# Kernel optimization log

Hardware: AMD Instinct MI355X
Metric: run time of the kernel (lower is better)

## Reference

```python
import jax, jax.numpy as jnp
import numpy as np

E = 8          # num_experts
K = 2          # top_k
R = 16         # lora_r
SCALING = 32.0 / 16.0  # lora_alpha / lora_r

B, S, H, I = 2, 2048, 2048, 8192


def setup_inputs() -> dict:
    key = jax.random.key(0)
    ks = jax.random.split(key, 11)
    inv_h = 1.0 / np.sqrt(H)
    inv_i = 1.0 / np.sqrt(I)
    return {
        "x": jax.random.normal(ks[0], (B, S, H), jnp.float32),
        "gate_W": jax.random.normal(ks[1], (I, H), jnp.float32) * inv_h,
        "up_W": jax.random.normal(ks[2], (I, H), jnp.float32) * inv_h,
        "down_W": jax.random.normal(ks[3], (H, I), jnp.float32) * inv_i,
        "router_W": jax.random.normal(ks[4], (E, H), jnp.float32) * 0.02,
        "gate_A": jax.random.normal(ks[5], (E, R, H), jnp.float32) * inv_h,
        "gate_B": jax.random.normal(ks[6], (E, I, R), jnp.float32) * 0.01,
        "up_A": jax.random.normal(ks[7], (E, R, H), jnp.float32) * inv_h,
        "up_B": jax.random.normal(ks[8], (E, I, R), jnp.float32) * 0.01,
        "down_A": jax.random.normal(ks[9], (E, R, I), jnp.float32) * inv_i,
        "down_B": jax.random.normal(ks[10], (E, H, R), jnp.float32) * 0.01,
    }


def _mixlora_forward(x, gate_W, up_W, down_W, router_W,
                     gate_A, gate_B, up_A, up_B, down_A, down_B):
    b, s, h = x.shape
    T = b * s
    xf = x.reshape(T, h)                                  # [T, H]

    # Shared base FFN projections (computed once for all experts)
    gate_out = xf @ gate_W.T                              # [T, I]
    up_out = xf @ up_W.T                                  # [T, I]

    # Router: softmax in fp32, top-k, renormalize selected weights
    logits = xf @ router_W.T                              # [T, E]
    probs = jax.nn.softmax(logits.astype(jnp.float32), axis=-1)
    w, idx = jax.lax.top_k(probs, K)                      # [T, K]
    w = w / jnp.sum(w, axis=-1, keepdims=True)

    # Dense per-(token, expert) combine weights; 0 for unselected experts
    onehot = jax.nn.one_hot(idx, E, dtype=probs.dtype)    # [T, K, E]
    w_dense = jnp.einsum('tke,tk->te', onehot, w)         # [T, E]

    # Load-balance aux loss: N * sum_i f_i * P_i
    f_i = jnp.sum(onehot, axis=(0, 1)) / T
    p_i = jnp.mean(probs, axis=0)
    aux_loss = E * jnp.dot(f_i, p_i)

    # Scan over experts, accumulating weighted intermediate and down-delta.
    # Since down_proj is linear, sum_k w_k * down(inter_k) = down(sum_k w_k * inter_k).
    def step(carry, p):
        acc_int, acc_dd = carry
        gA, gB, uA, uB, dA, dB, we = p                    # we: [T]
        gd = ((xf @ gA.T) @ gB.T) * SCALING               # [T, I]
        ud = ((xf @ uA.T) @ uB.T) * SCALING               # [T, I]
        inter = jax.nn.silu(gate_out + gd) * (up_out + ud)  # SwiGLU intermediate
        dd = ((inter @ dA.T) @ dB.T) * SCALING            # [T, H]
        we = we.astype(xf.dtype)[:, None]
        return (acc_int + we * inter, acc_dd + we * dd), None

    init = (jnp.zeros((T, gate_W.shape[0]), xf.dtype),
            jnp.zeros((T, h), xf.dtype))
    (acc_int, acc_dd), _ = jax.lax.scan(
        step, init, (gate_A, gate_B, up_A, up_B, down_A, down_B, w_dense.T))

    out = acc_int @ down_W.T + acc_dd                     # [T, H]
    return out.reshape(b, s, h), aux_loss


def reference(x, gate_W, up_W, down_W, router_W,
              gate_A, gate_B, up_A, up_B, down_A, down_B):
    return _mixlora_forward(x, gate_W, up_W, down_W, router_W,
                            gate_A, gate_B, up_A, up_B, down_A, down_B)
```

## Files before the change

### kernel.cpp

```cpp
#include <hip/hip_runtime.h>
#include <stdint.h>
#include <stddef.h>

#define DEVINL __device__ __forceinline__

typedef short sv8 __attribute__((ext_vector_type(8)));
typedef unsigned short usv8 __attribute__((ext_vector_type(8)));
typedef unsigned short usv4 __attribute__((ext_vector_type(4)));
typedef float f32x4 __attribute__((ext_vector_type(4)));

constexpr int T_TOK = 4096;
constexpr int H_DIM = 2048;
constexpr int I_DIM = 8192;
constexpr int E_NUM = 8;
constexpr int R_LORA = 16;
constexpr float SCALING = 2.0f;
constexpr int NQ = 4;
constexpr int TQ = T_TOK / NQ;
constexpr int PQ = TQ * 2;
constexpr int P_TOT = T_TOK * 2;

DEVINL float bf2f(unsigned short u) {
  union { uint32_t i; float f; } v; v.i = ((uint32_t)u) << 16; return v.f;
}
DEVINL unsigned short f2bf(float x) {
  union { float f; uint32_t i; } v; v.f = x;
  uint32_t r = v.i + 0x7FFFu + ((v.i >> 16) & 1u);
  return (unsigned short)(r >> 16);
}
DEVINL float bflo(uint32_t w) {
  union { uint32_t i; float f; } v; v.i = w << 16; return v.f;
}
DEVINL float bfhi(uint32_t w) {
  union { uint32_t i; float f; } v; v.i = w & 0xFFFF0000u; return v.f;
}

DEVINL f32x4 MFMA_BF16(sv8 a, sv8 b, f32x4 c) {
  return __builtin_amdgcn_mfma_f32_16x16x32_bf16(a, b, c, 0, 0, 0);
}

DEVINL void load16_to_lds(const void* g, void* l) {
  __builtin_amdgcn_global_load_lds(
      (const __attribute__((address_space(1))) uint32_t*)g,
      (__attribute__((address_space(3))) uint32_t*)l, 16, 0, 0);
}

#define BARRIER() __builtin_amdgcn_s_barrier()
#define SB0() __builtin_amdgcn_sched_barrier(0)
#define LGKM0() asm volatile("s_waitcnt lgkmcnt(0)" ::: "memory")

__global__ void cast_f32_to_bf16(const float4* __restrict__ src, usv4* __restrict__ dst) {
  long i = (long)blockIdx.x * blockDim.x + threadIdx.x;
  float4 v = src[i];
  usv4 o;
  o[0] = f2bf(v.x); o[1] = f2bf(v.y); o[2] = f2bf(v.z); o[3] = f2bf(v.w);
  dst[i] = o;
}

__global__ void zero_lcnt(int* lcnt) {
  if (threadIdx.x < E_NUM * NQ) lcnt[threadIdx.x] = 0;
}

__global__ void router_kernel(const float* __restrict__ x, const float* __restrict__ rW,
                              float* __restrict__ wbuf, int* __restrict__ idxb,
                              float* __restrict__ probs, int* __restrict__ lcnt,
                              int* __restrict__ lists, unsigned short* __restrict__ xf_bf) {
  const int wave = threadIdx.x >> 6, lane = threadIdx.x & 63;
  const int t = blockIdx.x * 4 + wave;
  const float* xr = x + (long)t * H_DIM;
  unsigned short* xbr = xf_bf + (long)t * H_DIM;
  float acc[E_NUM];
#pragma unroll
  for (int e = 0; e < E_NUM; ++e) acc[e] = 0.f;
  for (int h = lane; h < H_DIM; h += 64) {
    float xv = xr[h];
    xbr[h] = f2bf(xv);
#pragma unroll
    for (int e = 0; e < E_NUM; ++e) acc[e] += xv * rW[e * H_DIM + h];
  }
#pragma unroll
  for (int e = 0; e < E_NUM; ++e) {
#pragma unroll
    for (int off = 32; off; off >>= 1) acc[e] += __shfl_xor(acc[e], off);
  }
  if (lane == 0) {
    float mx = acc[0];
#pragma unroll
    for (int e = 1; e < E_NUM; ++e) mx = fmaxf(mx, acc[e]);
    float p[E_NUM];
    float s = 0.f;
#pragma unroll
    for (int e = 0; e < E_NUM; ++e) { p[e] = expf(acc[e] - mx); s += p[e]; }
    float inv = 1.f / s;
#pragma unroll
    for (int e = 0; e < E_NUM; ++e) p[e] *= inv;
    int e1 = 0;
    for (int e = 1; e < E_NUM; ++e) if (p[e] > p[e1]) e1 = e;
    int e2 = (e1 == 0) ? 1 : 0;
    for (int e = 0; e < E_NUM; ++e) if (e != e1 && p[e] > p[e2]) e2 = e;
    float w1 = p[e1], w2 = p[e2], wsum = w1 + w2;
    wbuf[t * 2 + 0] = w1 / wsum;
    wbuf[t * 2 + 1] = w2 / wsum;
    idxb[t * 2 + 0] = e1;
    idxb[t * 2 + 1] = e2;
#pragma unroll
    for (int e = 0; e < E_NUM; ++e) probs[(long)t * E_NUM + e] = p[e];
    const int q = t / TQ;
    int p1 = atomicAdd(&lcnt[e1 * NQ + q], 1); lists[(e1 * NQ + q) * TQ + p1] = t * 2 + 0;
    int p2 = atomicAdd(&lcnt[e2 * NQ + q], 1); lists[(e2 * NQ + q) * TQ + p2] = t * 2 + 1;
  }
}

__global__ void aux_kernel(const float* __restrict__ probs, const int* __restrict__ lcnt,
                           float* __restrict__ aux_out) {
  const int lane = threadIdx.x;
  float s[E_NUM];
#pragma unroll
  for (int e = 0; e < E_NUM; ++e) s[e] = 0.f;
  for (int t = lane; t < T_TOK; t += 64) {
#pragma unroll
    for (int e = 0; e < E_NUM; ++e) s[e] += probs[(long)t * E_NUM + e];
  }
#pragma unroll
  for (int e = 0; e < E_NUM; ++e) {
#pragma unroll
    for (int off = 32; off; off >>= 1) s[e] += __shfl_xor(s[e], off);
  }
  if (lane == 0) {
    float a = 0.f;
#pragma unroll
    for (int e = 0; e < E_NUM; ++e) {
      int cnt = 0;
#pragma unroll
      for (int q = 0; q < NQ; ++q) cnt += lcnt[e * NQ + q];
      a += ((float)cnt / (float)T_TOK) * (s[e] / (float)T_TOK);
    }
    *aux_out = (float)E_NUM * a;
  }
}

__global__ __launch_bounds__(256)
void lora_a_mfma_kernel(const unsigned short* __restrict__ xf_bf,
                        const unsigned short* __restrict__ gA_bf,
                        const unsigned short* __restrict__ uA_bf,
                        const int* __restrict__ lists, const int* __restrict__ lcnt,
                        float* __restrict__ vg, float* __restrict__ vu) {
  const int q = blockIdx.x / (E_NUM * 16);
  const int rem = blockIdx.x % (E_NUM * 16);
  const int e = rem >> 4;
  const int wave = threadIdx.x >> 6, lane = threadIdx.x & 63;
  const int grp = (rem & 15) * 4 + wave;
  const int npairs = lcnt[e * NQ + q];
  if (grp * 16 >= npairs) return;
  const int* lst = lists + (e * NQ + q) * TQ;
  const int slot = lane & 15;
  int pidx = grp * 16 + slot;
  int pair = lst[(pidx < npairs) ? pidx : grp * 16];
  int t = pair >> 1;
  const long kb = (long)blockIdx.y * 1024 + (lane >> 4) * 8;
  const unsigned short* arow = xf_bf + (long)t * H_DIM + kb;
  const unsigned short* bg = gA_bf + ((long)e * R_LORA + slot) * H_DIM + kb;
  const unsigned short* bu = uA_bf + ((long)e * R_LORA + slot) * H_DIM + kb;
  f32x4 ag = {}, au = {};
#pragma unroll 4
  for (int k = 0; k < 1024; k += 32) {
    sv8 a = *(const sv8*)(arow + k);
    ag = MFMA_BF16(a, *(const sv8*)(bg + k), ag);
    au = MFMA_BF16(a, *(const sv8*)(bu + k), au);
  }
  const int orow = (lane >> 4) * 4;
  const long base = (long)blockIdx.y * P_TOT;
#pragma unroll
  for (int rg = 0; rg < 4; ++rg) {
    int pidx2 = grp * 16 + orow + rg;
    if (pidx2 < npairs) {
      int pr = lst[pidx2];
      vg[(base + pr) * R_LORA + slot] = ag[rg];
      vu[(base + pr) * R_LORA + slot] = au[rg];
    }
  }
}

__global__ void reduce_uguu_kernel(const float* __restrict__ vg, const float* __restrict__ vu,
                                   float* __restrict__ ug, float* __restrict__ uu) {
  long i = (long)blockIdx.x * 256 + threadIdx.x;
  ug[i] = vg[i] + vg[(long)P_TOT * R_LORA + i];
  uu[i] = vu[i] + vu[(long)P_TOT * R_LORA + i];
}

__global__ __launch_bounds__(512, 2)
void gemm8p_kernel(const unsigned short* __restrict__ A,
                   const unsigned short* __restrict__ B0,
                   const unsigned short* __restrict__ B1,
                   unsigned short* __restrict__ C0,
                   unsigned short* __restrict__ C1,
                   int K, int ldc) {
  extern __shared__ unsigned short lds[];
  const unsigned short* __restrict__ B = blockIdx.z ? B1 : B0;
  unsigned short* __restrict__ C = blockIdx.z ? C1 : C0;
  const int tid = threadIdx.x;
  const int wave = tid >> 6, lane = tid & 63;
  const int wm = wave >> 2, wn = wave & 3;
  const long m0 = (long)blockIdx.y * 256;
  const long n0 = (long)blockIdx.x * 256;
  const int NT = K >> 6;

  const int lr = lane & 15;
  const int lc = (lane >> 4) * 8;
  const int xm = ((lane & 4) << 3) | ((lane & 2) << 3) | ((lane & 1) << 6);
  const int srow = tid >> 3;
  const int scol = (tid & 7) * 8;
  const int gcol = scol ^ (((tid >> 5) & 1) << 4) ^ (((tid >> 4) & 1) << 3)
                        ^ (((tid >> 3) & 1) << 5);

  f32x4 acc[8][4] = {};
  sv8 aF[4][2], bF[4][2];

  auto ldsAt = [&](int buf, int mat) -> unsigned short* {
    return lds + (((buf << 1) + mat) << 14);
  };
  auto stageA = [&](int buf, int R, long k0) {
    load16_to_lds(A + (m0 + R + srow) * K + k0 + gcol,
                  ldsAt(buf, 0) + ((R + srow) << 6) + scol);
  };
  auto stageB = [&](int buf, int R, long k0) {
    load16_to_lds(B + (n0 + R + srow) * K + k0 + gcol,
                  ldsAt(buf, 1) + ((R + srow) << 6) + scol);
  };
  auto rdA = [&](int buf, int row16, int ks) -> sv8 {
    int bo = ((((row16 + lr) << 7) + ((ks * 32 + lc) << 1))) ^ xm;
    return *(const sv8*)((const char*)ldsAt(buf, 0) + bo);
  };
  auto rdB = [&](int buf, int row16, int ks) -> sv8 {
    int bo = ((((row16 + lr) << 7) + ((ks * 32 + lc) << 1))) ^ xm;
    return *(const sv8*)((const char*)ldsAt(buf, 1) + bo);
  };

  stageA(0, 0, 0); stageA(0, 64, 0); stageA(0, 128, 0); stageA(0, 192, 0);
  stageB(0, 0, 0); stageB(0, 64, 0); stageB(0, 128, 0); stageB(0, 192, 0);
  if (NT > 1) {
    stageA(1, 0, 64); stageA(1, 128, 64);
    asm volatile("s_waitcnt vmcnt(2)" ::: "memory");
  } else {
    asm volatile("s_waitcnt vmcnt(0)" ::: "memory");
  }
  BARRIER();

  for (int t = 0; t < NT; ++t) {
    const int P = t & 1, Q = P ^ 1;
    const long kQ = ((long)t + 1) << 6;
    const long kP2 = ((long)t + 2) << 6;
    const bool hQ = (t + 1) < NT, hP2 = (t + 2) < NT;

#pragma unroll
    for (int mf = 0; mf < 4; ++mf)
#pragma unroll
      for (int ks = 0; ks < 2; ++ks)
        aF[mf][ks] = rdA(P, wm * 128 + mf * 16, ks);
#pragma unroll
    for (int nf = 0; nf < 2; ++nf)
#pragma unroll
      for (int ks = 0; ks < 2; ++ks)
        bF[nf][ks] = rdB(P, wn * 64 + nf * 16, ks);
    if (hQ) { stageA(Q, 64, kQ); stageA(Q, 192, kQ); }
    BARRIER(); LGKM0(); SB0();
    __builtin_amdgcn_s_setprio(1);
#pragma unroll
    for (int mf = 0; mf < 4; ++mf)
#pragma unroll
      for (int nf = 0; nf < 2; ++nf)
#pragma unroll
        for (int ks = 0; ks < 2; ++ks)
          acc[mf][nf] = MFMA_BF16(aF[mf][ks], bF[nf][ks], acc[mf][nf]);
    __builtin_amdgcn_s_setprio(0);
    BARRIER();

#pragma unroll
    for (int nf = 0; nf < 2; ++nf)
#pragma unroll
      for (int ks = 0; ks < 2; ++ks)
        bF[2 + nf][ks] = rdB(P, wn * 64 + (2 + nf) * 16, ks);
    if (hQ) { stageB(Q, 0, kQ); stageB(Q, 64, kQ); }
    BARRIER(); LGKM0(); SB0();
    __builtin_amdgcn_s_setprio(1);
#pragma unroll
    for (int mf = 0; mf < 4; ++mf)
#pragma unroll
      for (int nf = 0; nf < 2; ++nf)
#pragma unroll
        for (int ks = 0; ks < 2; ++ks)
          acc[mf][2 + nf] = MFMA_BF16(aF[mf][ks], bF[2 + nf][ks], acc[mf][2 + nf]);
    __builtin_amdgcn_s_setprio(0);
    BARRIER();

#pragma unroll
    for (int mf = 0; mf < 4; ++mf)
#pragma unroll
      for (int ks = 0; ks < 2; ++ks)
        aF[mf][ks] = rdA(P, wm * 128 + 64 + mf * 16, ks);
    if (hQ) { stageB(Q, 128, kQ); stageB(Q, 192, kQ); }
    BARRIER(); LGKM0(); SB0();
    __builtin_amdgcn_s_setprio(1);
#pragma unroll
    for (int mf = 0; mf < 4; ++mf)
#pragma unroll
      for (int nf = 0; nf < 2; ++nf)
#pragma unroll
        for (int ks = 0; ks < 2; ++ks)
          acc[4 + mf][nf] = MFMA_BF16(aF[mf][ks], bF[nf][ks], acc[4 + mf][nf]);
    __builtin_amdgcn_s_setprio(0);
    BARRIER();

    if (hP2) {
      stageA(P, 0, kP2); stageA(P, 128, kP2);
      asm volatile("s_waitcnt vmcnt(2)" ::: "memory");
    } else {
      asm volatile("s_waitcnt vmcnt(0)" ::: "memory");
    }
    BARRIER(); LGKM0(); SB0();
    __builtin_amdgcn_s_setprio(1);
#pragma unroll
    for (int mf = 0; mf < 4; ++mf)
#pragma unroll
      for (int nf = 0; nf < 2; ++nf)
#pragma unroll
        for (int ks = 0; ks < 2; ++ks)
          acc[4 + mf][2 + nf] = MFMA_BF16(aF[mf][ks], bF[2 + nf][ks], acc[4 + mf][2 + nf]);
    __builtin_amdgcn_s_setprio(0);
    BARRIER();
  }

  const int rb = (lane >> 4) * 4, cb = lane & 15;
#pragma unroll
  for (int mf = 0; mf < 8; ++mf)
#pragma unroll
    for (int nf = 0; nf < 4; ++nf) {
      long col = n0 + wn * 64 + nf * 16 + cb;
#pragma unroll
      for (int r = 0; r < 4; ++r) {
        long row = m0 + wm * 128 + mf * 16 + rb + r;
        C[row * ldc + col] = f2bf(acc[mf][nf][r]);
      }
    }
}

__global__ __launch_bounds__(256)
void combine2_kernel(const unsigned short* __restrict__ g_bf,
                     const unsigned short* __restrict__ u_bf,
                     const float* __restrict__ gB, const float* __restrict__ uB,
                     const float* __restrict__ ug, const float* __restrict__ uu,
                     const float* __restrict__ wbuf,
                     const int* __restrict__ lists, const int* __restrict__ lcnt,
                     unsigned short* __restrict__ winter, int q) {
  const int e = blockIdx.y >> 4, chunk = blockIdx.y & 15;
  const int npairs = lcnt[e * NQ + q];
  const int pbase = chunk * 64;
  if (pbase >= npairs) return;
  const int wave = threadIdx.x >> 6, lane = threadIdx.x & 63;
  const long i0 = (long)blockIdx.x * 256 + lane * 4;
  uint32_t gbp[32], ubp[32];
#pragma unroll
  for (int j = 0; j < 4; ++j) {
    const float4* gp = (const float4*)(gB + ((long)e * I_DIM + i0 + j) * R_LORA);
    const float4* up = (const float4*)(uB + ((long)e * I_DIM + i0 + j) * R_LORA);
#pragma unroll
    for (int c = 0; c < 4; ++c) {
      float4 gv = gp[c], uv = up[c];
      gbp[j * 8 + c * 2 + 0] = (uint32_t)f2bf(gv.x) | ((uint32_t)f2bf(gv.y) << 16);
      gbp[j * 8 + c * 2 + 1] = (uint32_t)f2bf(gv.z) | ((uint32_t)f2bf(gv.w) << 16);
      ubp[j * 8 + c * 2 + 0] = (uint32_t)f2bf(uv.x) | ((uint32_t)f2bf(uv.y) << 16);
      ubp[j * 8 + c * 2 + 1] = (uint32_t)f2bf(uv.z) | ((uint32_t)f2bf(uv.w) << 16);
    }
  }
  for (int pl = 0; pl < 16; ++pl) {
    int pi = pbase + wave + pl * 4;
    if (pi >= npairs) break;
    int pair = lists[(e * NQ + q) * TQ + pi];
    int t = pair >> 1, plocal = pair - q * PQ;
    float w = wbuf[pair];
    const float2* ug2 = (const float2*)(ug + (long)pair * R_LORA);
    const float2* uu2 = (const float2*)(uu + (long)pair * R_LORA);
    usv4 gv = *(const usv4*)(g_bf + (long)t * I_DIM + i0);
    usv4 uv = *(const usv4*)(u_bf + (long)t * I_DIM + i0);
    float gd[4] = {0.f, 0.f, 0.f, 0.f}, ud[4] = {0.f, 0.f, 0.f, 0.f};
#pragma unroll
    for (int c = 0; c < 8; ++c) {
      float2 a = ug2[c], b = uu2[c];
#pragma unroll
      for (int j = 0; j < 4; ++j) {
        uint32_t gw = gbp[j * 8 + c], uw = ubp[j * 8 + c];
        gd[j] += a.x * bflo(gw) + a.y * bfhi(gw);
        ud[j] += b.x * bflo(uw) + b.y * bfhi(uw);
      }
    }
    usv4 o;
#pragma unroll
    for (int j = 0; j < 4; ++j) {
      float zg = bf2f(gv[j]) + SCALING * gd[j];
      float zu = bf2f(uv[j]) + SCALING * ud[j];
      float sil = zg / (1.f + __expf(-zg));
      o[j] = f2bf(w * sil * zu);
    }
    *(usv4*)(winter + (long)plocal * I_DIM + i0) = o;
  }
}

__global__ void acc_kernel(const unsigned short* __restrict__ winter,
                           unsigned short* __restrict__ acc_bf, int q) {
  long gid = (long)blockIdx.x * 256 + threadIdx.x;
  int tl = (int)(gid >> 10);
  int ig = (int)(gid & 1023);
  int t = q * TQ + tl;
  usv8 a = *(const usv8*)(winter + ((long)(tl * 2 + 0)) * I_DIM + ig * 8);
  usv8 b = *(const usv8*)(winter + ((long)(tl * 2 + 1)) * I_DIM + ig * 8);
  usv8 o;
#pragma unroll
  for (int j = 0; j < 8; ++j) o[j] = f2bf(bf2f(a[j]) + bf2f(b[j]));
  *(usv8*)(acc_bf + (long)t * I_DIM + ig * 8) = o;
}

__global__ __launch_bounds__(256)
void lorav_mfma_kernel(const unsigned short* __restrict__ winter,
                       const unsigned short* __restrict__ dA_bf,
                       const int* __restrict__ lists, const int* __restrict__ lcnt,
                       float* __restrict__ vv, int q) {
  const int e = blockIdx.x >> 4;
  const int wave = threadIdx.x >> 6, lane = threadIdx.x & 63;
  const int grp = (blockIdx.x & 15) * 4 + wave;
  const int npairs = lcnt[e * NQ + q];
  if (grp * 16 >= npairs) return;
  const int* lst = lists + (e * NQ + q) * TQ;
  const int slot = lane & 15;
  int pidx = grp * 16 + slot;
  int pair = lst[(pidx < npairs) ? pidx : grp * 16];
  int plocal = pair - q * PQ;
  const long kb = (long)blockIdx.y * 1024 + (lane >> 4) * 8;
  const unsigned short* arow = winter + (long)plocal * I_DIM + kb;
  const unsigned short* brow = dA_bf + ((long)e * R_LORA + slot) * I_DIM + kb;
  f32x4 acc = {};
#pragma unroll 4
  for (int k = 0; k < 1024; k += 32)
    acc = MFMA_BF16(*(const sv8*)(arow + k), *(const sv8*)(brow + k), acc);
  const int orow = (lane >> 4) * 4;
  const long base = (long)blockIdx.y * P_TOT;
#pragma unroll
  for (int rg = 0; rg < 4; ++rg) {
    int pidx2 = grp * 16 + orow + rg;
    if (pidx2 < npairs) {
      int pr = lst[pidx2];
      vv[(base + pr) * R_LORA + slot] = acc[rg];
    }
  }
}

__global__ void reduce_v_kernel(const float* __restrict__ vv, float* __restrict__ vbuf) {
  long i = (long)blockIdx.x * 256 + threadIdx.x;
  float s = 0.f;
#pragma unroll
  for (int kc = 0; kc < 8; ++kc) s += vv[(long)kc * P_TOT * R_LORA + i];
  vbuf[i] = s;
}

__global__ void dd_kernel(const float* __restrict__ vbuf, const int* __restrict__ idxb,
                          const float* __restrict__ dB,
                          float* __restrict__ out) {
  const int t = blockIdx.y;
  const int h = blockIdx.x * 256 + threadIdx.x;
  const int e0 = idxb[t * 2 + 0], e1 = idxb[t * 2 + 1];
  const float4* v0p = (const float4*)(vbuf + (long)(t * 2 + 0) * R_LORA);
  const float4* v1p = (const float4*)(vbuf + (long)(t * 2 + 1) * R_LORA);
  const float4* b0 = (const float4*)(dB + ((long)e0 * H_DIM + h) * R_LORA);
  const float4* b1 = (const float4*)(dB + ((long)e1 * H_DIM + h) * R_LORA);
  float dd = 0.f;
#pragma unroll
  for (int qq = 0; qq < 4; ++qq) {
    float4 v0 = v0p[qq], x0 = b0[qq];
    float4 v1 = v1p[qq], x1 = b1[qq];
    dd += v0.x * x0.x + v0.y * x0.y + v0.z * x0.z + v0.w * x0.w;
    dd += v1.x * x1.x + v1.y * x1.y + v1.z * x1.z + v1.w * x1.w;
  }
  out[(long)t * H_DIM + h] = SCALING * dd;
}

__global__ __launch_bounds__(256, 2)
void gemm2_kernel(const unsigned short* __restrict__ A,
                  const unsigned short* __restrict__ B,
                  float* __restrict__ out) {
  constexpr int Kd = I_DIM;
  __shared__ unsigned short As[128 * 32];
  __shared__ unsigned short Bs[128 * 32];
  const int tid = threadIdx.x;
  const int wave = tid >> 6, lane = tid & 63;
  const int wm = wave >> 1, wn = wave & 1;
  const long m0 = (long)blockIdx.y * 128;
  const long n0 = (long)blockIdx.x * 128;
  f32x4 acc[4][4] = {};
  const int srow = wave * 32 + (lane >> 2);
  const int scol = (lane & 3) * 8;
  const unsigned short* Ag = A + (m0 + srow) * Kd + scol;
  const unsigned short* Bg = B + (n0 + srow) * Kd + scol;
  const int frA = wm * 64 + (lane & 15);
  const int frB = wn * 64 + (lane & 15);
  const int fc = (lane >> 4) * 8;

  for (int k0 = 0; k0 < Kd; k0 += 32) {
    __syncthreads();
#pragma unroll
    for (int c = 0; c < 2; ++c) {
      load16_to_lds(Ag + (long)c * 16 * Kd + k0, &As[(wave * 32 + c * 16) * 32]);
      load16_to_lds(Bg + (long)c * 16 * Kd + k0, &Bs[(wave * 32 + c * 16) * 32]);
    }
    __syncthreads();
    sv8 af[4], bf[4];
#pragma unroll
    for (int m = 0; m < 4; ++m) af[m] = *(const sv8*)&As[(frA + m * 16) * 32 + fc];
#pragma unroll
    for (int n = 0; n < 4; ++n) bf[n] = *(const sv8*)&Bs[(frB + n * 16) * 32 + fc];
#pragma unroll
    for (int m = 0; m < 4; ++m)
#pragma unroll
      for (int n = 0; n < 4; ++n) acc[m][n] = MFMA_BF16(af[m], bf[n], acc[m][n]);
  }

  const int rb = (lane >> 4) * 4, cb = lane & 15;
#pragma unroll
  for (int m = 0; m < 4; ++m)
#pragma unroll
    for (int n = 0; n < 4; ++n) {
      long col = n0 + wn * 64 + n * 16 + cb;
#pragma unroll
      for (int r = 0; r < 4; ++r) {
        long row = m0 + wm * 64 + m * 16 + rb + r;
        out[row * H_DIM + col] += acc[m][n][r];
      }
    }
}

extern "C" void kernel_launch(void* const* d_in, const int* in_sizes, int n_in,
                              void* d_out, int out_size, void* d_ws, size_t ws_size,
                              hipStream_t stream) {
  (void)in_sizes; (void)n_in; (void)out_size;
  const float* x        = (const float*)d_in[0];
  const float* gate_W   = (const float*)d_in[1];
  const float* up_W     = (const float*)d_in[2];
  const float* down_W   = (const float*)d_in[3];
  const float* router_W = (const float*)d_in[4];
  const float* gate_A   = (const float*)d_in[5];
  const float* gate_B   = (const float*)d_in[6];
  const float* up_A     = (const float*)d_in[7];
  const float* up_B     = (const float*)d_in[8];
  const float* down_A   = (const float*)d_in[9];
  const float* down_B   = (const float*)d_in[10];
  float* out = (float*)d_out;

  char* ws = (char*)d_ws;
  size_t off = 0;
  auto take = [&](size_t bytes) -> char* {
    char* p = ws + off;
    off += (bytes + 255) & ~(size_t)255;
    return p;
  };
  unsigned short* xf_bf  = (unsigned short*)take((size_t)T_TOK * H_DIM * 2);
  unsigned short* gW_bf  = (unsigned short*)take((size_t)I_DIM * H_DIM * 2);
  unsigned short* uW_bf  = (unsigned short*)take((size_t)I_DIM * H_DIM * 2);
  unsigned short* dA_bf  = (unsigned short*)take((size_t)E_NUM * R_LORA * I_DIM * 2);
  unsigned short* g_bf   = (unsigned short*)take((size_t)T_TOK * I_DIM * 2);
  unsigned short* u_bf   = (unsigned short*)take((size_t)T_TOK * I_DIM * 2);
  unsigned short* winterQ= (unsigned short*)take((size_t)PQ * I_DIM * 2);
  float* wbuf  = (float*)take((size_t)P_TOT * 4);
  int*   idxb  = (int*)take((size_t)P_TOT * 4);
  float* ug    = (float*)take((size_t)P_TOT * R_LORA * 4);
  float* uu    = (float*)take((size_t)P_TOT * R_LORA * 4);
  float* vbuf  = (float*)take((size_t)P_TOT * R_LORA * 4);
  float* probs = (float*)take((size_t)T_TOK * E_NUM * 4);
  int*   lcnt  = (int*)take((size_t)E_NUM * NQ * 4);
  int*   lists = (int*)take((size_t)E_NUM * NQ * TQ * 4);

  unsigned short* dW_bf  = gW_bf;
  unsigned short* acc_bf = g_bf;
  float* vg = (float*)winterQ;
  float* vu = (float*)(winterQ + (size_t)1 * 1024 * 1024 / 2);
  unsigned short* gA_bf = winterQ + (size_t)2 * 1024 * 1024 / 2;
  unsigned short* uA_bf = winterQ + (size_t)5 * 512 * 1024 / 2;
  float* vv = (float*)xf_bf;

  if (ws_size < off) return;

  zero_lcnt<<<1, 64, 0, stream>>>(lcnt);
  router_kernel<<<T_TOK / 4, 256, 0, stream>>>(x, router_W, wbuf, idxb, probs, lcnt, lists, xf_bf);
  aux_kernel<<<1, 64, 0, stream>>>(probs, lcnt, out + (size_t)T_TOK * H_DIM);

  cast_f32_to_bf16<<<(E_NUM * R_LORA * H_DIM / 4) / 256, 256, 0, stream>>>((const float4*)gate_A, (usv4*)gA_bf);
  cast_f32_to_bf16<<<(E_NUM * R_LORA * H_DIM / 4) / 256, 256, 0, stream>>>((const float4*)up_A, (usv4*)uA_bf);
  lora_a_mfma_kernel<<<dim3(NQ * E_NUM * 16, 2), 256, 0, stream>>>(xf_bf, gA_bf, uA_bf, lists, lcnt, vg, vu);
  reduce_uguu_kernel<<<(P_TOT * R_LORA) / 256, 256, 0, stream>>>(vg, vu, ug, uu);

  cast_f32_to_bf16<<<(I_DIM * H_DIM / 4) / 256, 256, 0, stream>>>((const float4*)gate_W, (usv4*)gW_bf);
  cast_f32_to_bf16<<<(I_DIM * H_DIM / 4) / 256, 256, 0, stream>>>((const float4*)up_W, (usv4*)uW_bf);
  cast_f32_to_bf16<<<(E_NUM * R_LORA * I_DIM / 4) / 256, 256, 0, stream>>>((const float4*)down_A, (usv4*)dA_bf);

  hipFuncSetAttribute((const void*)gemm8p_kernel,
                      hipFuncAttributeMaxDynamicSharedMemorySize, 131072);
  gemm8p_kernel<<<dim3(I_DIM / 256, T_TOK / 256, 2), 512, 131072, stream>>>(
      xf_bf, gW_bf, uW_bf, g_bf, u_bf, H_DIM, I_DIM);

  cast_f32_to_bf16<<<(H_DIM * I_DIM / 4) / 256, 256, 0, stream>>>((const float4*)down_W, (usv4*)dW_bf);

  for (int q = 0; q < NQ; ++q) {
    combine2_kernel<<<dim3(I_DIM / 256, E_NUM * 16), 256, 0, stream>>>(
        g_bf, u_bf, gate_B, up_B, ug, uu, wbuf, lists, lcnt, winterQ, q);
    acc_kernel<<<(TQ * (I_DIM / 8)) / 256, 256, 0, stream>>>(winterQ, acc_bf, q);
    lorav_mfma_kernel<<<dim3(E_NUM * 16, 8), 256, 0, stream>>>(winterQ, dA_bf, lists, lcnt, vv, q);
  }
  reduce_v_kernel<<<(P_TOT * R_LORA) / 256, 256, 0, stream>>>(vv, vbuf);

  dd_kernel<<<dim3(H_DIM / 256, T_TOK), 256, 0, stream>>>(vbuf, idxb, down_B, out);
  gemm2_kernel<<<dim3(H_DIM / 128, T_TOK / 128), 256, 0, stream>>>(acc_bf, dW_bf, out);
}
```

Before: 1.176 ms.

## Reuse pipelined 256x256 GEMM with split-K for down projection

Generalizes the pipelined 256x256 MFMA GEMM into a template that takes explicit strides, per-z offsets and an optional fp32 output. It then replaces the simple 128x128 down-projection GEMM with this kernel using split-K over two halves of I, followed by a merge kernel that adds both partials into the output. The point is to give the down GEMM the better LDS pipelining and enough blocks to fill the device, at the cost of an extra fp32 partial buffer and a merge pass. It also drops the explicit lgkmcnt waits and sched barriers after the barriers, which is a risky change to the LDS read ordering.

```diff
diff --git a/kernel.cpp b/kernel.cpp
--- a/kernel.cpp
+++ b/kernel.cpp
@@ -46,8 +46,6 @@
 }
 
 #define BARRIER() __builtin_amdgcn_s_barrier()
-#define SB0() __builtin_amdgcn_sched_barrier(0)
-#define LGKM0() asm volatile("s_waitcnt lgkmcnt(0)" ::: "memory")
 
 __global__ void cast_f32_to_bf16(const float4* __restrict__ src, usv4* __restrict__ dst) {
   long i = (long)blockIdx.x * blockDim.x + threadIdx.x;
@@ -188,16 +186,20 @@
   uu[i] = vu[i] + vu[(long)P_TOT * R_LORA + i];
 }
 
+template <bool F32OUT>
 __global__ __launch_bounds__(512, 2)
-void gemm8p_kernel(const unsigned short* __restrict__ A,
-                   const unsigned short* __restrict__ B0,
-                   const unsigned short* __restrict__ B1,
-                   unsigned short* __restrict__ C0,
-                   unsigned short* __restrict__ C1,
-                   int K, int ldc) {
+void gemm8p_t(const unsigned short* __restrict__ A,
+              const unsigned short* __restrict__ B0,
+              const unsigned short* __restrict__ B1,
+              unsigned short* __restrict__ Cb0,
+              unsigned short* __restrict__ Cb1,
+              float* __restrict__ Cf,
+              int K, int lda, int ldb, int ldc,
+              int az_off, int bz_off, long cz_off) {
   extern __shared__ unsigned short lds[];
-  const unsigned short* __restrict__ B = blockIdx.z ? B1 : B0;
-  unsigned short* __restrict__ C = blockIdx.z ? C1 : C0;
+  const int z = blockIdx.z;
+  const unsigned short* __restrict__ Ap = A + (long)z * az_off;
+  const unsigned short* __restrict__ Bp = (z ? B1 : B0) + (long)z * bz_off;
   const int tid = threadIdx.x;
   const int wave = tid >> 6, lane = tid & 63;
   const int wm = wave >> 2, wn = wave & 3;
@@ -220,11 +222,11 @@
     return lds + (((buf << 1) + mat) << 14);
   };
   auto stageA = [&](int buf, int R, long k0) {
-    load16_to_lds(A + (m0 + R + srow) * K + k0 + gcol,
+    load16_to_lds(Ap + (m0 + R + srow) * (long)lda + k0 + gcol,
                   ldsAt(buf, 0) + ((R + srow) << 6) + scol);
   };
   auto stageB = [&](int buf, int R, long k0) {
-    load16_to_lds(B + (n0 + R + srow) * K + k0 + gcol,
+    load16_to_lds(Bp + (n0 + R + srow) * (long)ldb + k0 + gcol,
                   ldsAt(buf, 1) + ((R + srow) << 6) + scol);
   };
   auto rdA = [&](int buf, int row16, int ks) -> sv8 {
@@ -263,7 +265,7 @@
       for (int ks = 0; ks < 2; ++ks)
         bF[nf][ks] = rdB(P, wn * 64 + nf * 16, ks);
     if (hQ) { stageA(Q, 64, kQ); stageA(Q, 192, kQ); }
-    BARRIER(); LGKM0(); SB0();
+    BARRIER();
     __builtin_amdgcn_s_setprio(1);
 #pragma unroll
     for (int mf = 0; mf < 4; ++mf)
@@ -281,7 +283,7 @@
       for (int ks = 0; ks < 2; ++ks)
         bF[2 + nf][ks] = rdB(P, wn * 64 + (2 + nf) * 16, ks);
     if (hQ) { stageB(Q, 0, kQ); stageB(Q, 64, kQ); }
-    BARRIER(); LGKM0(); SB0();
+    BARRIER();
     __builtin_amdgcn_s_setprio(1);
 #pragma unroll
     for (int mf = 0; mf < 4; ++mf)
@@ -299,7 +301,7 @@
       for (int ks = 0; ks < 2; ++ks)
         aF[mf][ks] = rdA(P, wm * 128 + 64 + mf * 16, ks);
     if (hQ) { stageB(Q, 128, kQ); stageB(Q, 192, kQ); }
-    BARRIER(); LGKM0(); SB0();
+    BARRIER();
     __builtin_amdgcn_s_setprio(1);
 #pragma unroll
     for (int mf = 0; mf < 4; ++mf)
@@ -317,7 +319,7 @@
     } else {
       asm volatile("s_waitcnt vmcnt(0)" ::: "memory");
     }
-    BARRIER(); LGKM0(); SB0();
+    BARRIER();
     __builtin_amdgcn_s_setprio(1);
 #pragma unroll
     for (int mf = 0; mf < 4; ++mf)
@@ -331,17 +333,33 @@
   }
 
   const int rb = (lane >> 4) * 4, cb = lane & 15;
-#pragma unroll
-  for (int mf = 0; mf < 8; ++mf)
-#pragma unroll
-    for (int nf = 0; nf < 4; ++nf) {
-      long col = n0 + wn * 64 + nf * 16 + cb;
-#pragma unroll
-      for (int r = 0; r < 4; ++r) {
-        long row = m0 + wm * 128 + mf * 16 + rb + r;
-        C[row * ldc + col] = f2bf(acc[mf][nf][r]);
+  if constexpr (F32OUT) {
+    float* __restrict__ Cp = Cf + (long)z * cz_off;
+#pragma unroll
+    for (int mf = 0; mf < 8; ++mf)
+#pragma unroll
+      for (int nf = 0; nf < 4; ++nf) {
+        long col = n0 + wn * 64 + nf * 16 + cb;
+#pragma unroll
+        for (int r = 0; r < 4; ++r) {
+          long row = m0 + wm * 128 + mf * 16 + rb + r;
+          Cp[row * ldc + col] = acc[mf][nf][r];
+        }
       }
-    }
+  } else {
+    unsigned short* __restrict__ Cp = z ? Cb1 : Cb0;
+#pragma unroll
+    for (int mf = 0; mf < 8; ++mf)
+#pragma unroll
+      for (int nf = 0; nf < 4; ++nf) {
+        long col = n0 + wn * 64 + nf * 16 + cb;
+#pragma unroll
+        for (int r = 0; r < 4; ++r) {
+          long row = m0 + wm * 128 + mf * 16 + rb + r;
+          Cp[row * ldc + col] = f2bf(acc[mf][nf][r]);
+        }
+      }
+  }
 }
 
 __global__ __launch_bounds__(256)
@@ -482,58 +500,12 @@
   out[(long)t * H_DIM + h] = SCALING * dd;
 }
 
-__global__ __launch_bounds__(256, 2)
-void gemm2_kernel(const unsigned short* __restrict__ A,
-                  const unsigned short* __restrict__ B,
-                  float* __restrict__ out) {
-  constexpr int Kd = I_DIM;
-  __shared__ unsigned short As[128 * 32];
-  __shared__ unsigned short Bs[128 * 32];
-  const int tid = threadIdx.x;
-  const int wave = tid >> 6, lane = tid & 63;
-  const int wm = wave >> 1, wn = wave & 1;
-  const long m0 = (long)blockIdx.y * 128;
-  const long n0 = (long)blockIdx.x * 128;
-  f32x4 acc[4][4] = {};
-  const int srow = wave * 32 + (lane >> 2);
-  const int scol = (lane & 3) * 8;
-  const unsigned short* Ag = A + (m0 + srow) * Kd + scol;
-  const unsigned short* Bg = B + (n0 + srow) * Kd + scol;
-  const int frA = wm * 64 + (lane & 15);
-  const int frB = wn * 64 + (lane & 15);
-  const int fc = (lane >> 4) * 8;
-
-  for (int k0 = 0; k0 < Kd; k0 += 32) {
-    __syncthreads();
-#pragma unroll
-    for (int c = 0; c < 2; ++c) {
-      load16_to_lds(Ag + (long)c * 16 * Kd + k0, &As[(wave * 32 + c * 16) * 32]);
-      load16_to_lds(Bg + (long)c * 16 * Kd + k0, &Bs[(wave * 32 + c * 16) * 32]);
-    }
-    __syncthreads();
-    sv8 af[4], bf[4];
-#pragma unroll
-    for (int m = 0; m < 4; ++m) af[m] = *(const sv8*)&As[(frA + m * 16) * 32 + fc];
-#pragma unroll
-    for (int n = 0; n < 4; ++n) bf[n] = *(const sv8*)&Bs[(frB + n * 16) * 32 + fc];
-#pragma unroll
-    for (int m = 0; m < 4; ++m)
-#pragma unroll
-      for (int n = 0; n < 4; ++n) acc[m][n] = MFMA_BF16(af[m], bf[n], acc[m][n]);
-  }
-
-  const int rb = (lane >> 4) * 4, cb = lane & 15;
-#pragma unroll
-  for (int m = 0; m < 4; ++m)
-#pragma unroll
-    for (int n = 0; n < 4; ++n) {
-      long col = n0 + wn * 64 + n * 16 + cb;
-#pragma unroll
-      for (int r = 0; r < 4; ++r) {
-        long row = m0 + wm * 64 + m * 16 + rb + r;
-        out[row * H_DIM + col] += acc[m][n][r];
-      }
-    }
+__global__ void merge_out_kernel(const float4* __restrict__ p0, const float4* __restrict__ p1,
+                                 float4* __restrict__ out) {
+  long i = (long)blockIdx.x * 256 + threadIdx.x;
+  float4 a = p0[i], b = p1[i], o = out[i];
+  o.x += a.x + b.x; o.y += a.y + b.y; o.z += a.z + b.z; o.w += a.w + b.w;
+  out[i] = o;
 }
 
 extern "C" void kernel_launch(void* const* d_in, const int* in_sizes, int n_in,
@@ -583,6 +555,7 @@
   unsigned short* gA_bf = winterQ + (size_t)2 * 1024 * 1024 / 2;
   unsigned short* uA_bf = winterQ + (size_t)5 * 512 * 1024 / 2;
   float* vv = (float*)xf_bf;
+  float* pbuf = (float*)u_bf;
 
   if (ws_size < off) return;
 
@@ -599,10 +572,13 @@
   cast_f32_to_bf16<<<(I_DIM * H_DIM / 4) / 256, 256, 0, stream>>>((const float4*)up_W, (usv4*)uW_bf);
   cast_f32_to_bf16<<<(E_NUM * R_LORA * I_DIM / 4) / 256, 256, 0, stream>>>((const float4*)down_A, (usv4*)dA_bf);
 
-  hipFuncSetAttribute((const void*)gemm8p_kernel,
+  hipFuncSetAttribute(reinterpret_cast<const void*>(&gemm8p_t<false>),
                       hipFuncAttributeMaxDynamicSharedMemorySize, 131072);
-  gemm8p_kernel<<<dim3(I_DIM / 256, T_TOK / 256, 2), 512, 131072, stream>>>(
-      xf_bf, gW_bf, uW_bf, g_bf, u_bf, H_DIM, I_DIM);
+  hipFuncSetAttribute(reinterpret_cast<const void*>(&gemm8p_t<true>),
+                      hipFuncAttributeMaxDynamicSharedMemorySize, 131072);
+  gemm8p_t<false><<<dim3(I_DIM / 256, T_TOK / 256, 2), 512, 131072, stream>>>(
+      xf_bf, gW_bf, uW_bf, g_bf, u_bf, nullptr,
+      H_DIM, H_DIM, H_DIM, I_DIM, 0, 0, 0);
 
   cast_f32_to_bf16<<<(H_DIM * I_DIM / 4) / 256, 256, 0, stream>>>((const float4*)down_W, (usv4*)dW_bf);
 
@@ -615,5 +591,10 @@
   reduce_v_kernel<<<(P_TOT * R_LORA) / 256, 256, 0, stream>>>(vv, vbuf);
 
   dd_kernel<<<dim3(H_DIM / 256, T_TOK), 256, 0, stream>>>(vbuf, idxb, down_B, out);
-  gemm2_kernel<<<dim3(H_DIM / 128, T_TOK / 128), 256, 0, stream>>>(acc_bf, dW_bf, out);
-}
+
+  gemm8p_t<true><<<dim3(H_DIM / 256, T_TOK / 256, 2), 512, 131072, stream>>>(
+      acc_bf, dW_bf, dW_bf, nullptr, nullptr, pbuf,
+      I_DIM / 2, I_DIM, I_DIM, H_DIM, I_DIM / 2, I_DIM / 2, (long)T_TOK * H_DIM);
+  merge_out_kernel<<<(T_TOK * H_DIM / 4) / 256, 256, 0, stream>>>(
+      (const float4*)pbuf, (const float4*)(pbuf + (size_t)T_TOK * H_DIM), (float4*)out);
+}
```

Measured after the change: 1.152 ms. 1.02x faster.
